# Kernel optimization log

Hardware: AMD Instinct MI355X
Metric: run time of the kernel (lower is better)

Reference implementation:

```python
import jax, jax.numpy as jnp
import numpy as np

H = 1024
S = 2048
B = 16


def setup_inputs() -> dict:
    key = jax.random.key(0)
    ks = jax.random.split(key, 8)
    scale = 1.0 / np.sqrt(H)
    return {
        "a": jax.random.normal(ks[0], (S, H), dtype=jnp.float32),
        "b": jax.random.normal(ks[1], (B, S, H), dtype=jnp.float32),
        "Wa": jax.random.normal(ks[2], (H, H), dtype=jnp.float32) * scale,
        "ba": jax.random.normal(ks[3], (H,), dtype=jnp.float32) * scale,
        "Wb": jax.random.normal(ks[4], (H, H), dtype=jnp.float32) * scale,
        "bb": jax.random.normal(ks[5], (H,), dtype=jnp.float32) * scale,
        "wc": jax.random.normal(ks[6], (H,), dtype=jnp.float32) * scale,
        "bc": jax.random.normal(ks[7], (), dtype=jnp.float32) * scale,
    }


def reference(a, b, Wa, ba, Wb, bb, wc, bc):
    # a: [S, H], b: [B, S, H]; weights stored as [H_in, H_out]
    pa = a @ Wa + ba                     # [S, H]
    pb = jnp.einsum('bsh,hk->bsk', b, Wb) + bb  # [B, S, H]
    # additive attention score: linearc((pa + pb)) -> [B, S]
    scores = jnp.einsum('bsh,h->bs', pa[None] + pb, wc) + bc
    att = jax.nn.softmax(scores, axis=-1)       # softmax over S (as in source)
    # weighted sum over dim 0 (B)
    return jnp.einsum('bs,bsh->sh', att, b)     # [S, H]
```

## Files before the change

kernel.cpp:

```cpp
#include <hip/hip_runtime.h>
#include <math.h>

#define H 1024
#define S 2048
#define B 16

__device__ inline float wave_reduce_sum(float x) {
    #pragma unroll
    for (int off = 32; off > 0; off >>= 1)
        x += __shfl_down(x, off, 64);
    return x;
}
__device__ inline float wave_reduce_max(float x) {
    #pragma unroll
    for (int off = 32; off > 0; off >>= 1)
        x = fmaxf(x, __shfl_down(x, off, 64));
    return x;
}

__device__ inline float row_dot(const float* __restrict__ Mr,
                                const float* __restrict__ vec, int lane) {
    float acc = 0.f;
    #pragma unroll
    for (int k = lane * 4; k < H; k += 64 * 4) {
        float4 m4 = *reinterpret_cast<const float4*>(Mr + k);
        float4 v4 = *reinterpret_cast<const float4*>(vec + k);
        acc += m4.x * v4.x + m4.y * v4.y + m4.z * v4.z + m4.w * v4.w;
    }
    return wave_reduce_sum(acc);
}

__global__ void uv_kernel(const float* __restrict__ Wa,
                          const float* __restrict__ Wb,
                          const float* __restrict__ wc,
                          float* __restrict__ u, float* __restrict__ v) {
    const int lane = threadIdx.x & 63;
    const int wid  = threadIdx.x >> 6;
    const int row  = blockIdx.x * (blockDim.x >> 6) + wid;
    const float* Mr = (row < H) ? (Wa + (size_t)row * H) : (Wb + (size_t)(row - H) * H);
    float acc = row_dot(Mr, wc, lane);
    if (lane == 0) {
        if (row < H) u[row] = acc; else v[row - H] = acc;
    }
}

__global__ void scores_kernel(const float* __restrict__ a,
                              const float* __restrict__ bmat,
                              const float* __restrict__ u,
                              const float* __restrict__ v,
                              float* __restrict__ sa,
                              float* __restrict__ raw) {
    const int lane = threadIdx.x & 63;
    const int wid  = threadIdx.x >> 6;
    const int row  = blockIdx.x * (blockDim.x >> 6) + wid;
    const bool is_a = (row < S);
    const float* Mr  = is_a ? (a + (size_t)row * H) : (bmat + (size_t)(row - S) * H);
    const float* vec = is_a ? u : v;
    float acc = row_dot(Mr, vec, lane);
    if (lane == 0) {
        if (is_a) sa[row] = acc; else raw[row - S] = acc;
    }
}

__global__ void stats_kernel(const float* __restrict__ raw,
                             const float* __restrict__ sa,
                             float* __restrict__ stats) {
    const int b    = blockIdx.x;
    const int lane = threadIdx.x & 63;
    const int wid  = threadIdx.x >> 6;
    __shared__ float sred[4];

    float vals[8];
    float m = -INFINITY;
    #pragma unroll
    for (int i = 0; i < 8; i++) {
        int s = threadIdx.x + i * 256;
        vals[i] = raw[b * S + s] + sa[s];
        m = fmaxf(m, vals[i]);
    }
    m = wave_reduce_max(m);
    if (lane == 0) sred[wid] = m;
    __syncthreads();
    m = fmaxf(fmaxf(sred[0], sred[1]), fmaxf(sred[2], sred[3]));
    __syncthreads();

    float sum = 0.f;
    #pragma unroll
    for (int i = 0; i < 8; i++) sum += expf(vals[i] - m);
    sum = wave_reduce_sum(sum);
    if (lane == 0) sred[wid] = sum;
    __syncthreads();
    if (threadIdx.x == 0) {
        float den = sred[0] + sred[1] + sred[2] + sred[3];
        stats[2 * b]     = m;
        stats[2 * b + 1] = 1.0f / den;
    }
}

__global__ void wsum_kernel(const float* __restrict__ bmat,
                            const float* __restrict__ raw,
                            const float* __restrict__ sa,
                            const float* __restrict__ stats,
                            float* __restrict__ out) {
    const int s = blockIdx.x;
    __shared__ float att[B];
    if (threadIdx.x < B) {
        const int b = threadIdx.x;
        att[b] = expf(raw[b * S + s] + sa[s] - stats[2 * b]) * stats[2 * b + 1];
    }
    __syncthreads();

    const int t = threadIdx.x;
    const float4* bp = reinterpret_cast<const float4*>(bmat) + (size_t)s * (H / 4) + t;
    float4 acc = make_float4(0.f, 0.f, 0.f, 0.f);
    #pragma unroll
    for (int b = 0; b < B; b++) {
        const float w = att[b];
        const float4 x = bp[(size_t)b * (S * (H / 4))];
        acc.x += w * x.x;
        acc.y += w * x.y;
        acc.z += w * x.z;
        acc.w += w * x.w;
    }
    reinterpret_cast<float4*>(out)[(size_t)s * (H / 4) + t] = acc;
}

extern "C" void kernel_launch(void* const* d_in, const int* in_sizes, int n_in,
                              void* d_out, int out_size, void* d_ws, size_t ws_size,
                              hipStream_t stream) {
    const float* a  = (const float*)d_in[0];
    const float* bm = (const float*)d_in[1];
    const float* Wa = (const float*)d_in[2];
    const float* Wb = (const float*)d_in[4];
    const float* wc = (const float*)d_in[6];
    float* out = (float*)d_out;

    float* ws    = (float*)d_ws;
    float* u     = ws;
    float* v     = ws + 1024;
    float* sa    = ws + 2048;
    float* raw   = ws + 4096;
    float* stats = ws + 4096 + B * S;

    uv_kernel<<<2048 / 4, 256, 0, stream>>>(Wa, Wb, wc, u, v);
    scores_kernel<<<(S + B * S) / 4, 256, 0, stream>>>(a, bm, u, v, sa, raw);
    stats_kernel<<<B, 256, 0, stream>>>(raw, sa, stats);
    wsum_kernel<<<S, 256, 0, stream>>>(bm, raw, sa, stats, out);
}
```

Baseline: 61.17 us.

## Fuse softmax stats into score kernel via unnormalized exp and atomic partial sums

Removes the separate stats kernel. The score kernel now processes one sequence position per block, computing all 16 batch scores plus the a-row score, then writing exp(score) without max subtraction and atomically adding it into 64-way striped partial denominators. The weighted-sum kernel reduces those partials and normalizes. This saves a launch and a round trip through the raw scores, and keeps the weight vectors in registers. It adds a memset and atomics, and dropping the max subtraction risks overflow for large scores.

```diff
diff --git a/kernel.cpp b/kernel.cpp
--- a/kernel.cpp
+++ b/kernel.cpp
@@ -11,107 +11,90 @@
         x += __shfl_down(x, off, 64);
     return x;
 }
-__device__ inline float wave_reduce_max(float x) {
-    #pragma unroll
-    for (int off = 32; off > 0; off >>= 1)
-        x = fmaxf(x, __shfl_down(x, off, 64));
-    return x;
-}
 
-__device__ inline float row_dot(const float* __restrict__ Mr,
-                                const float* __restrict__ vec, int lane) {
+__device__ inline float row_dot_reg(const float4* __restrict__ Mr4,
+                                    const float4* vr, int lane) {
     float acc = 0.f;
     #pragma unroll
-    for (int k = lane * 4; k < H; k += 64 * 4) {
-        float4 m4 = *reinterpret_cast<const float4*>(Mr + k);
-        float4 v4 = *reinterpret_cast<const float4*>(vec + k);
-        acc += m4.x * v4.x + m4.y * v4.y + m4.z * v4.z + m4.w * v4.w;
+    for (int i = 0; i < 4; i++) {
+        float4 m4 = Mr4[lane + i * 64];
+        acc += m4.x * vr[i].x + m4.y * vr[i].y + m4.z * vr[i].z + m4.w * vr[i].w;
     }
     return wave_reduce_sum(acc);
 }
 
-__global__ void uv_kernel(const float* __restrict__ Wa,
-                          const float* __restrict__ Wb,
-                          const float* __restrict__ wc,
-                          float* __restrict__ u, float* __restrict__ v) {
+__global__ __launch_bounds__(256)
+void uv_kernel(const float* __restrict__ Wa, const float* __restrict__ Wb,
+               const float* __restrict__ wc,
+               float* __restrict__ u, float* __restrict__ v) {
     const int lane = threadIdx.x & 63;
     const int wid  = threadIdx.x >> 6;
-    const int row  = blockIdx.x * (blockDim.x >> 6) + wid;
-    const float* Mr = (row < H) ? (Wa + (size_t)row * H) : (Wb + (size_t)(row - H) * H);
-    float acc = row_dot(Mr, wc, lane);
-    if (lane == 0) {
-        if (row < H) u[row] = acc; else v[row - H] = acc;
+    const int row  = blockIdx.x * 4 + wid;
+    const float4* w4 = reinterpret_cast<const float4*>(wc);
+    float4 wr[4];
+    #pragma unroll
+    for (int i = 0; i < 4; i++) wr[i] = w4[lane + i * 64];
+    const float* Mr = (row < H) ? (Wa + (size_t)row * H)
+                                : (Wb + (size_t)(row - H) * H);
+    float acc = row_dot_reg(reinterpret_cast<const float4*>(Mr), wr, lane);
+    if (lane == 0) { if (row < H) u[row] = acc; else v[row - H] = acc; }
+}
+
+__global__ __launch_bounds__(256)
+void score_kernel(const float* __restrict__ a, const float* __restrict__ bmat,
+                  const float* __restrict__ u, const float* __restrict__ v,
+                  float* __restrict__ e, float* __restrict__ den_part) {
+    const int lane = threadIdx.x & 63;
+    const int wid  = threadIdx.x >> 6;
+    const int s    = blockIdx.x;
+    __shared__ float raw_s[17];
+
+    const float4* v4 = reinterpret_cast<const float4*>(v);
+    float4 vr[4];
+    #pragma unroll
+    for (int i = 0; i < 4; i++) vr[i] = v4[lane + i * 64];
+
+    #pragma unroll
+    for (int r = wid; r < 16; r += 4) {
+        const float4* Mr4 =
+            reinterpret_cast<const float4*>(bmat + ((size_t)r * S + s) * H);
+        float d = row_dot_reg(Mr4, vr, lane);
+        if (lane == 0) raw_s[r] = d;
+    }
+    if (wid == 0) {
+        const float4* u4 = reinterpret_cast<const float4*>(u);
+        float4 ur[4];
+        #pragma unroll
+        for (int i = 0; i < 4; i++) ur[i] = u4[lane + i * 64];
+        float d = row_dot_reg(reinterpret_cast<const float4*>(a + (size_t)s * H),
+                              ur, lane);
+        if (lane == 0) raw_s[16] = d;
+    }
+    __syncthreads();
+    if (threadIdx.x < B) {
+        const int b = threadIdx.x;
+        float ev = expf(raw_s[b] + raw_s[16]);
+        e[(size_t)s * B + b] = ev;
+        atomicAdd(&den_part[b * 64 + (blockIdx.x & 63)], ev);
     }
 }
 
-__global__ void scores_kernel(const float* __restrict__ a,
-                              const float* __restrict__ bmat,
-                              const float* __restrict__ u,
-                              const float* __restrict__ v,
-                              float* __restrict__ sa,
-                              float* __restrict__ raw) {
-    const int lane = threadIdx.x & 63;
-    const int wid  = threadIdx.x >> 6;
-    const int row  = blockIdx.x * (blockDim.x >> 6) + wid;
-    const bool is_a = (row < S);
-    const float* Mr  = is_a ? (a + (size_t)row * H) : (bmat + (size_t)(row - S) * H);
-    const float* vec = is_a ? u : v;
-    float acc = row_dot(Mr, vec, lane);
-    if (lane == 0) {
-        if (is_a) sa[row] = acc; else raw[row - S] = acc;
-    }
-}
-
-__global__ void stats_kernel(const float* __restrict__ raw,
-                             const float* __restrict__ sa,
-                             float* __restrict__ stats) {
-    const int b    = blockIdx.x;
-    const int lane = threadIdx.x & 63;
-    const int wid  = threadIdx.x >> 6;
-    __shared__ float sred[4];
-
-    float vals[8];
-    float m = -INFINITY;
-    #pragma unroll
-    for (int i = 0; i < 8; i++) {
-        int s = threadIdx.x + i * 256;
-        vals[i] = raw[b * S + s] + sa[s];
-        m = fmaxf(m, vals[i]);
-    }
-    m = wave_reduce_max(m);
-    if (lane == 0) sred[wid] = m;
-    __syncthreads();
-    m = fmaxf(fmaxf(sred[0], sred[1]), fmaxf(sred[2], sred[3]));
-    __syncthreads();
-
-    float sum = 0.f;
-    #pragma unroll
-    for (int i = 0; i < 8; i++) sum += expf(vals[i] - m);
-    sum = wave_reduce_sum(sum);
-    if (lane == 0) sred[wid] = sum;
-    __syncthreads();
-    if (threadIdx.x == 0) {
-        float den = sred[0] + sred[1] + sred[2] + sred[3];
-        stats[2 * b]     = m;
-        stats[2 * b + 1] = 1.0f / den;
-    }
-}
-
-__global__ void wsum_kernel(const float* __restrict__ bmat,
-                            const float* __restrict__ raw,
-                            const float* __restrict__ sa,
-                            const float* __restrict__ stats,
-                            float* __restrict__ out) {
+__global__ __launch_bounds__(256)
+void wsum_kernel(const float* __restrict__ bmat, const float* __restrict__ e,
+                 const float* __restrict__ den_part, float* __restrict__ out) {
     const int s = blockIdx.x;
     __shared__ float att[B];
     if (threadIdx.x < B) {
         const int b = threadIdx.x;
-        att[b] = expf(raw[b * S + s] + sa[s] - stats[2 * b]) * stats[2 * b + 1];
+        float den = 0.f;
+        #pragma unroll
+        for (int j = 0; j < 64; j++) den += den_part[b * 64 + j];
+        att[b] = e[(size_t)s * B + b] / den;
     }
     __syncthreads();
-
     const int t = threadIdx.x;
-    const float4* bp = reinterpret_cast<const float4*>(bmat) + (size_t)s * (H / 4) + t;
+    const float4* bp = reinterpret_cast<const float4*>(bmat)
+                       + (size_t)s * (H / 4) + t;
     float4 acc = make_float4(0.f, 0.f, 0.f, 0.f);
     #pragma unroll
     for (int b = 0; b < B; b++) {
@@ -135,15 +118,15 @@
     const float* wc = (const float*)d_in[6];
     float* out = (float*)d_out;
 
-    float* ws    = (float*)d_ws;
-    float* u     = ws;
-    float* v     = ws + 1024;
-    float* sa    = ws + 2048;
-    float* raw   = ws + 4096;
-    float* stats = ws + 4096 + B * S;
+    float* ws       = (float*)d_ws;
+    float* u        = ws;
+    float* v        = ws + 1024;
+    float* e        = ws + 2048;
+    float* den_part = ws + 2048 + S * B;
+
+    hipMemsetAsync(den_part, 0, B * 64 * sizeof(float), stream);
 
     uv_kernel<<<2048 / 4, 256, 0, stream>>>(Wa, Wb, wc, u, v);
-    scores_kernel<<<(S + B * S) / 4, 256, 0, stream>>>(a, bm, u, v, sa, raw);
-    stats_kernel<<<B, 256, 0, stream>>>(raw, sa, stats);
-    wsum_kernel<<<S, 256, 0, stream>>>(bm, raw, sa, stats, out);
+    score_kernel<<<S, 256, 0, stream>>>(a, bm, u, v, e, den_part);
+    wsum_kernel<<<S, 256, 0, stream>>>(bm, e, den_part, out);
 }
```

New measurement: 65.89 us. 1.08x slower.
